# Kernel optimization log

Hardware: AMD Instinct MI355X
Metric: run time of the kernel (lower is better)

## Reference

```python
import jax, jax.numpy as jnp
import numpy as np

D_MODEL = 1024
N_HEADS = 16
D_K = D_MODEL // N_HEADS


def setup_inputs() -> dict:
    key = jax.random.key(0)
    k1, k2, k3, k4, k5 = jax.random.split(key, 5)
    B, S = 2, 2048
    scale = 1.0 / np.sqrt(D_MODEL)
    return {
        "query": jax.random.normal(k1, (B, S, D_MODEL), dtype=jnp.float32),
        "mask": jnp.ones((B, S, S), dtype=jnp.int32),
        "W_qkv": jax.random.normal(k2, (D_MODEL, 3 * D_MODEL), dtype=jnp.float32) * scale,
        "b_qkv": jax.random.normal(k3, (3 * D_MODEL,), dtype=jnp.float32) * 0.02,
        "W_out": jax.random.normal(k4, (D_MODEL, D_MODEL), dtype=jnp.float32) * scale,
        "b_out": jax.random.normal(k5, (D_MODEL,), dtype=jnp.float32) * 0.02,
    }


def reference(query, mask, W_qkv, b_qkv, W_out, b_out):
    B, S, _ = query.shape
    # fused QKV projection (all from query, matching the torch module)
    qkv = query @ W_qkv + b_qkv                      # [B, S, 3*D]
    q, k, v = jnp.split(qkv, 3, axis=-1)
    # [B, H, S, d_k]
    q = q.reshape(B, S, N_HEADS, D_K).transpose(0, 2, 1, 3)
    k = k.reshape(B, S, N_HEADS, D_K).transpose(0, 2, 1, 3)
    v = v.reshape(B, S, N_HEADS, D_K).transpose(0, 2, 1, 3)
    # scaled dot-product attention with explicit scores
    scores = jnp.einsum("bhqd,bhkd->bhqk", q, k) / jnp.sqrt(jnp.float32(D_K))
    m = mask[:, None, :, :]                           # [B, 1, S, S] broadcast over heads
    scores = jnp.where(m == 0, jnp.float32(-1e9), scores)
    attn = jax.nn.softmax(scores, axis=-1)           # dropout p=0 in eval -> identity
    ctx = jnp.einsum("bhqk,bhkd->bhqd", attn, v)     # [B, H, S, d_k]
    ctx = ctx.transpose(0, 2, 1, 3).reshape(B, S, D_MODEL)
    return ctx @ W_out + b_out
```

## Files before the change

kernel.cpp:

```cpp
#include <hip/hip_runtime.h>
#include <stdint.h>
#include <stddef.h>

#define S_LEN 2048
#define NB    2
#define DM    1024
#define NH    16
#define DKH   64
#define NTOK  4096
#define QKV_N 3072
#define QSCALE 0.18033688f

typedef __attribute__((ext_vector_type(4))) float floatx4;
using half2v = __attribute__((ext_vector_type(2))) _Float16;
using half4v = __attribute__((ext_vector_type(4))) _Float16;
using half8v = __attribute__((ext_vector_type(8))) _Float16;
using fp16x2 = __attribute__((ext_vector_type(2))) __fp16;

#if __has_builtin(__builtin_amdgcn_exp2f)
#define EXP2F __builtin_amdgcn_exp2f
#else
#define EXP2F exp2f
#endif

#define WAITCNT_VM8() asm volatile("s_waitcnt vmcnt(8)" ::: "memory")
#define WAITCNT_VM0() asm volatile("s_waitcnt vmcnt(0)" ::: "memory")
#define BARRIER_RAW() asm volatile("s_barrier" ::: "memory")

__device__ __forceinline__ void glds16(const void* g, void* l) {
    __builtin_amdgcn_global_load_lds((const __attribute__((address_space(1))) void*)g,
                                     (__attribute__((address_space(3))) void*)l,
                                     16, 0, 0);
}

__global__ __launch_bounds__(256) void prep_kernel(const float* __restrict__ query,
                                                   _Float16* __restrict__ qh,
                                                   const float* __restrict__ Wqkv,
                                                   _Float16* __restrict__ wqt,
                                                   const float* __restrict__ Wout,
                                                   _Float16* __restrict__ wot,
                                                   const int* __restrict__ mask,
                                                   int* __restrict__ flag) {
    __shared__ float tbuf[32][33];
    constexpr int CAST_B = NTOK * DM / 4 / 256;
    constexpr int TQ_B   = (QKV_N / 32) * (DM / 32);
    constexpr int TO_B   = (DM / 32) * (DM / 32);
    const int bid = blockIdx.x;

    if (bid < CAST_B) {
        int i = bid * 256 + threadIdx.x;
        float4 v = ((const float4*)query)[i];
        half4v o = {(_Float16)v.x, (_Float16)v.y, (_Float16)v.z, (_Float16)v.w};
        ((half4v*)qh)[i] = o;
    } else if (bid < CAST_B + TQ_B + TO_B) {
        const float* in; _Float16* out; int C, t;
        if (bid < CAST_B + TQ_B) { t = bid - CAST_B;        in = Wqkv; out = wqt; C = QKV_N; }
        else                     { t = bid - CAST_B - TQ_B; in = Wout; out = wot; C = DM;    }
        const int R = DM;
        int c0 = (t % (C / 32)) * 32, r0 = (t / (C / 32)) * 32;
        int x = threadIdx.x & 31, y0 = threadIdx.x >> 5;
        #pragma unroll
        for (int k = 0; k < 4; ++k) {
            int y = y0 + k * 8;
            tbuf[y][x] = in[(size_t)(r0 + y) * C + c0 + x];
        }
        __syncthreads();
        #pragma unroll
        for (int k = 0; k < 4; ++k) {
            int y = y0 + k * 8;
            out[(size_t)(c0 + y) * R + r0 + x] = (_Float16)tbuf[x][y];
        }
    } else {
        int i = (bid - CAST_B - TQ_B - TO_B) * 256 + threadIdx.x;
        int4 v = ((const int4*)mask)[i];
        if ((v.x == 0) | (v.y == 0) | (v.z == 0) | (v.w == 0)) *flag = 0;
    }
}

template <int FINAL, int BN>
__global__ __launch_bounds__(256) void gemm_bt_kernel(const _Float16* __restrict__ A,
                                                      const _Float16* __restrict__ Bt,
                                                      const float* __restrict__ bias,
                                                      float* __restrict__ Cf,
                                                      _Float16* __restrict__ Ch,
                                                      _Float16* __restrict__ Vt,
                                                      int M, int N, int K) {
    constexpr int NJ = BN / 32;
    __shared__ _Float16 As[128 * 64];
    __shared__ _Float16 Bs[BN * 64];

    const int nt = blockIdx.x, mt = blockIdx.y;
    const int tid = threadIdx.x, wave = tid >> 6, lane = tid & 63;
    const int quad = lane >> 4, l16 = lane & 15;
    const int wm = wave >> 1, wn = wave & 1;

    floatx4 acc[4][NJ];
    #pragma unroll
    for (int i = 0; i < 4; ++i)
        #pragma unroll
        for (int j = 0; j < NJ; ++j)
            #pragma unroll
            for (int r = 0; r < 4; ++r) acc[i][j][r] = 0.0f;

    const _Float16* Ab = A + (size_t)mt * 128 * K;
    const _Float16* Bb = Bt + (size_t)nt * BN * K;

    for (int kt = 0; kt < K; kt += 64) {
        #pragma unroll
        for (int p = 0; p < 4; ++p) {
            int slot = p * 256 + wave * 64 + lane;
            int row = slot >> 3, cc = slot & 7, c = cc ^ (row & 7);
            glds16(Ab + (size_t)row * K + kt + c * 8, As + (size_t)(p * 256 + wave * 64) * 8);
        }
        #pragma unroll
        for (int p = 0; p < BN / 32; ++p) {
            int slot = p * 256 + wave * 64 + lane;
            int row = slot >> 3, cc = slot & 7, c = cc ^ (row & 7);
            glds16(Bb + (size_t)row * K + kt + c * 8, Bs + (size_t)(p * 256 + wave * 64) * 8);
        }
        __syncthreads();

        #pragma unroll
        for (int kk = 0; kk < 2; ++kk) {
            half8v af[4], bfr[NJ];
            #pragma unroll
            for (int i = 0; i < 4; ++i) {
                int row = wm * 64 + i * 16 + l16;
                int c = (kk * 4 + quad) ^ (row & 7);
                af[i] = *(const half8v*)(As + row * 64 + c * 8);
            }
            #pragma unroll
            for (int j = 0; j < NJ; ++j) {
                int row = wn * (BN / 2) + j * 16 + l16;
                int c = (kk * 4 + quad) ^ (row & 7);
                bfr[j] = *(const half8v*)(Bs + row * 64 + c * 8);
            }
            #pragma unroll
            for (int i = 0; i < 4; ++i)
                #pragma unroll
                for (int j = 0; j < NJ; ++j)
                    acc[i][j] = __builtin_amdgcn_mfma_f32_16x16x32_f16(af[i], bfr[j], acc[i][j], 0, 0, 0);
        }
        __syncthreads();
    }

    #pragma unroll
    for (int j = 0; j < NJ; ++j) {
        int n = nt * BN + wn * (BN / 2) + j * 16 + l16;
        float bv = bias[n];
        #pragma unroll
        for (int i = 0; i < 4; ++i) {
            int m0 = mt * 128 + wm * 64 + i * 16 + quad * 4;
            float v[4];
            #pragma unroll
            for (int r = 0; r < 4; ++r) v[r] = acc[i][j][r] + bv;
            if (FINAL) {
                #pragma unroll
                for (int r = 0; r < 4; ++r) Cf[(size_t)(m0 + r) * N + n] = v[r];
            } else {
                if (n < DM) {
                    #pragma unroll
                    for (int r = 0; r < 4; ++r) v[r] *= QSCALE;
                }
                if (n < 2 * DM) {
                    #pragma unroll
                    for (int r = 0; r < 4; ++r)
                        Ch[(size_t)(m0 + r) * QKV_N + n] = (_Float16)v[r];
                } else {
                    int bb = m0 >> 11, s = m0 & (S_LEN - 1);
                    half4v t = {(_Float16)v[0], (_Float16)v[1], (_Float16)v[2], (_Float16)v[3]};
                    *(half4v*)(Vt + ((size_t)bb * (NH * DKH) + (n - 2 * DM)) * S_LEN + s) = t;
                }
            }
        }
    }
}

__global__ __launch_bounds__(256) void flash_kernel(const _Float16* __restrict__ qkv,
                                                    const _Float16* __restrict__ vt,
                                                    const int* __restrict__ mask,
                                                    const int* __restrict__ flag,
                                                    _Float16* __restrict__ ctx) {
    __shared__ _Float16 Ks[2 * 128 * 64];
    __shared__ _Float16 Vs[2 * 64 * 128];

    const int bh = blockIdx.x, qt = blockIdx.y;
    const int b = bh >> 4, h = bh & 15;
    const int tid = threadIdx.x, wave = tid >> 6, lane = tid & 63;
    const int quad = lane >> 4, l16 = lane & 15;
    const int allones = (*flag != 0);

    const _Float16* qrow0 = qkv + (size_t)(b * S_LEN + qt * 128 + wave * 32 + l16) * QKV_N + h * DKH;
    const _Float16* qrow1 = qrow0 + (size_t)16 * QKV_N;
    half8v qa0 = *(const half8v*)(qrow0 + quad * 8);
    half8v qa1 = *(const half8v*)(qrow0 + 32 + quad * 8);
    half8v qb0 = *(const half8v*)(qrow1 + quad * 8);
    half8v qb1 = *(const half8v*)(qrow1 + 32 + quad * 8);
    WAITCNT_VM0();

    const _Float16* kbase = qkv + (size_t)b * S_LEN * QKV_N + DM + h * DKH;
    const _Float16* vbase = vt + (size_t)(b * NH + h) * DKH * S_LEN;

    auto stage = [&](int buf, int kt) {
        #pragma unroll
        for (int p = 0; p < 4; ++p) {
            int slot = p * 256 + wave * 64 + lane;
            int row = slot >> 3, cc = slot & 7, c = cc ^ (row & 7);
            glds16(kbase + (size_t)(kt * 128 + row) * QKV_N + c * 8,
                   Ks + buf * (128 * 64) + (size_t)(p * 256 + wave * 64) * 8);
        }
        #pragma unroll
        for (int p = 0; p < 4; ++p) {
            int slot = p * 256 + wave * 64 + lane;
            int row = slot >> 4, cc = slot & 15, c = cc ^ (row & 15);
            glds16(vbase + (size_t)row * S_LEN + kt * 128 + c * 8,
                   Vs + buf * (64 * 128) + (size_t)(p * 256 + wave * 64) * 8);
        }
    };

    floatx4 oa[4], ob[4];
    #pragma unroll
    for (int c = 0; c < 4; ++c)
        #pragma unroll
        for (int r = 0; r < 4; ++r) { oa[c][r] = 0.0f; ob[c][r] = 0.0f; }
    float lsa = 0.0f, lsb = 0.0f;

    stage(0, 0);

    for (int kt = 0; kt < S_LEN / 128; ++kt) {
        const int cur = kt & 1;
        if (kt < S_LEN / 128 - 1) {
            stage(cur ^ 1, kt + 1);
            WAITCNT_VM8();
        } else {
            WAITCNT_VM0();
        }
        BARRIER_RAW();

        const _Float16* Ksb = Ks + cur * (128 * 64);
        const _Float16* Vsb = Vs + cur * (64 * 128);

        half4v pa[8], pb[8];
        #pragma unroll
        for (int j = 0; j < 8; ++j) {
            int rowk = j * 16 + l16;
            half8v a0 = *(const half8v*)(Ksb + rowk * 64 + ((quad) ^ (rowk & 7)) * 8);
            half8v a1 = *(const half8v*)(Ksb + rowk * 64 + ((4 + quad) ^ (rowk & 7)) * 8);
            floatx4 za, zb;
            #pragma unroll
            for (int r = 0; r < 4; ++r) { za[r] = 0.0f; zb[r] = 0.0f; }
            __builtin_amdgcn_s_setprio(1);
            za = __builtin_amdgcn_mfma_f32_16x16x32_f16(a0, qa0, za, 0, 0, 0);
            za = __builtin_amdgcn_mfma_f32_16x16x32_f16(a1, qa1, za, 0, 0, 0);
            zb = __builtin_amdgcn_mfma_f32_16x16x32_f16(a0, qb0, zb, 0, 0, 0);
            zb = __builtin_amdgcn_mfma_f32_16x16x32_f16(a1, qb1, zb, 0, 0, 0);
            __builtin_amdgcn_s_setprio(0);

            if (!allones) {
                for (int r = 0; r < 4; ++r) {
                    int s = kt * 128 + j * 16 + quad * 4 + r;
                    int qA = qt * 128 + wave * 32 + l16;
                    if (mask[((size_t)b * S_LEN + qA) * S_LEN + s] == 0) za[r] = -1e9f;
                    if (mask[((size_t)b * S_LEN + qA + 16) * S_LEN + s] == 0) zb[r] = -1e9f;
                }
            }

            float p0 = EXP2F(za[0]), p1 = EXP2F(za[1]), p2 = EXP2F(za[2]), p3 = EXP2F(za[3]);
            lsa += (p0 + p1) + (p2 + p3);
            fp16x2 lo = __builtin_amdgcn_cvt_pkrtz(p0, p1);
            fp16x2 hi = __builtin_amdgcn_cvt_pkrtz(p2, p3);
            half2v lo2 = __builtin_bit_cast(half2v, lo);
            half2v hi2 = __builtin_bit_cast(half2v, hi);
            half4v pka = {lo2.x, lo2.y, hi2.x, hi2.y};
            pa[j] = pka;

            p0 = EXP2F(zb[0]); p1 = EXP2F(zb[1]); p2 = EXP2F(zb[2]); p3 = EXP2F(zb[3]);
            lsb += (p0 + p1) + (p2 + p3);
            lo = __builtin_amdgcn_cvt_pkrtz(p0, p1);
            hi = __builtin_amdgcn_cvt_pkrtz(p2, p3);
            lo2 = __builtin_bit_cast(half2v, lo);
            hi2 = __builtin_bit_cast(half2v, hi);
            half4v pkb = {lo2.x, lo2.y, hi2.x, hi2.y};
            pb[j] = pkb;
        }

        #pragma unroll
        for (int j = 0; j < 8; ++j) {
            int g = 2 * j + (quad >> 1);
            __builtin_amdgcn_s_setprio(1);
            #pragma unroll
            for (int c = 0; c < 4; ++c) {
                int rowv = c * 16 + l16;
                half4v bv = *(const half4v*)(Vsb + rowv * 128 + ((g ^ (rowv & 15)) * 8) + (quad & 1) * 4);
                oa[c] = __builtin_amdgcn_mfma_f32_16x16x16f16(pa[j], bv, oa[c], 0, 0, 0);
                ob[c] = __builtin_amdgcn_mfma_f32_16x16x16f16(pb[j], bv, ob[c], 0, 0, 0);
            }
            __builtin_amdgcn_s_setprio(0);
        }

        if (kt < S_LEN / 128 - 1) BARRIER_RAW();
    }

    lsa += __shfl_xor(lsa, 16); lsa += __shfl_xor(lsa, 32);
    lsb += __shfl_xor(lsb, 16); lsb += __shfl_xor(lsb, 32);
    float lia[4], lib[4];
    #pragma unroll
    for (int r = 0; r < 4; ++r) {
        int src = (lane & 48) | ((lane >> 4) * 4 + r);
        lia[r] = 1.0f / __shfl(lsa, src);
        lib[r] = 1.0f / __shfl(lsb, src);
    }

    #pragma unroll
    for (int c = 0; c < 4; ++c)
        #pragma unroll
        for (int r = 0; r < 4; ++r) {
            int qA = qt * 128 + wave * 32 + quad * 4 + r;
            int col = h * DKH + c * 16 + l16;
            ctx[(size_t)(b * S_LEN + qA) * DM + col]      = (_Float16)(oa[c][r] * lia[r]);
            ctx[(size_t)(b * S_LEN + qA + 16) * DM + col] = (_Float16)(ob[c][r] * lib[r]);
        }
}

extern "C" void kernel_launch(void* const* d_in, const int* in_sizes, int n_in,
                              void* d_out, int out_size, void* d_ws, size_t ws_size,
                              hipStream_t stream) {
    const float* query = (const float*)d_in[0];
    const int*   mask  = (const int*)d_in[1];
    const float* W_qkv = (const float*)d_in[2];
    const float* b_qkv = (const float*)d_in[3];
    const float* W_out = (const float*)d_in[4];
    const float* b_out = (const float*)d_in[5];
    float* out = (float*)d_out;

    char* w = (char*)d_ws;
    _Float16* qh   = (_Float16*)w;  w += (size_t)NTOK * DM * 2;
    _Float16* wqt  = (_Float16*)w;  w += (size_t)QKV_N * DM * 2;
    _Float16* wot  = (_Float16*)w;  w += (size_t)DM * DM * 2;
    _Float16* qkvh = (_Float16*)w;  w += (size_t)NTOK * QKV_N * 2;
    _Float16* vt   = (_Float16*)w;  w += (size_t)NB * NH * DKH * S_LEN * 2;
    int*      flag = (int*)w;
    _Float16* ctxh = qh;

    hipMemsetAsync(flag, 1, 4, stream);

    constexpr int PREP_BLOCKS = (NTOK * DM / 4 / 256)
                              + (QKV_N / 32) * (DM / 32)
                              + (DM / 32) * (DM / 32)
                              + (NB * S_LEN * S_LEN / 4 / 256);
    prep_kernel<<<PREP_BLOCKS, 256, 0, stream>>>(query, qh, W_qkv, wqt, W_out, wot, mask, flag);

    gemm_bt_kernel<0, 128><<<dim3(QKV_N / 128, NTOK / 128), 256, 0, stream>>>(
        qh, wqt, b_qkv, nullptr, qkvh, vt, NTOK, QKV_N, DM);

    flash_kernel<<<dim3(NB * NH, S_LEN / 128), 256, 0, stream>>>(qkvh, vt, mask, flag, ctxh);

    gemm_bt_kernel<1, 64><<<dim3(DM / 64, NTOK / 128), 256, 0, stream>>>(
        ctxh, wot, b_out, out, nullptr, nullptr, NTOK, DM, DM);
}
```

Baseline: 213.3 us.

## Split flash attention work across 8 waves with 16 query rows each

The flash kernel moves from 4 waves handling 32 query rows each to 8 waves handling 16 rows each, with 512 threads per block. The K/V tile staging is spread over twice as many threads, so each thread issues half as many async loads, and the vmcnt wait is adjusted to match. The s_setprio hints are dropped. This aims to raise occupancy and latency hiding, at the cost of each wave reusing a K/V fragment for only one query tile instead of two, which doubles LDS reads per MFMA.

```diff
diff --git a/kernel.cpp b/kernel.cpp
--- a/kernel.cpp
+++ b/kernel.cpp
@@ -23,7 +23,7 @@
 #define EXP2F exp2f
 #endif
 
-#define WAITCNT_VM8() asm volatile("s_waitcnt vmcnt(8)" ::: "memory")
+#define WAITCNT_VM4() asm volatile("s_waitcnt vmcnt(4)" ::: "memory")
 #define WAITCNT_VM0() asm volatile("s_waitcnt vmcnt(0)" ::: "memory")
 #define BARRIER_RAW() asm volatile("s_barrier" ::: "memory")
 
@@ -176,11 +176,11 @@
     }
 }
 
-__global__ __launch_bounds__(256) void flash_kernel(const _Float16* __restrict__ qkv,
-                                                    const _Float16* __restrict__ vt,
-                                                    const int* __restrict__ mask,
-                                                    const int* __restrict__ flag,
-                                                    _Float16* __restrict__ ctx) {
+__global__ __launch_bounds__(512, 4) void flash_kernel(const _Float16* __restrict__ qkv,
+                                                       const _Float16* __restrict__ vt,
+                                                       const int* __restrict__ mask,
+                                                       const int* __restrict__ flag,
+                                                       _Float16* __restrict__ ctx) {
     __shared__ _Float16 Ks[2 * 128 * 64];
     __shared__ _Float16 Vs[2 * 64 * 128];
 
@@ -190,12 +190,9 @@
     const int quad = lane >> 4, l16 = lane & 15;
     const int allones = (*flag != 0);
 
-    const _Float16* qrow0 = qkv + (size_t)(b * S_LEN + qt * 128 + wave * 32 + l16) * QKV_N + h * DKH;
-    const _Float16* qrow1 = qrow0 + (size_t)16 * QKV_N;
+    const _Float16* qrow0 = qkv + (size_t)(b * S_LEN + qt * 128 + wave * 16 + l16) * QKV_N + h * DKH;
     half8v qa0 = *(const half8v*)(qrow0 + quad * 8);
     half8v qa1 = *(const half8v*)(qrow0 + 32 + quad * 8);
-    half8v qb0 = *(const half8v*)(qrow1 + quad * 8);
-    half8v qb1 = *(const half8v*)(qrow1 + 32 + quad * 8);
     WAITCNT_VM0();
 
     const _Float16* kbase = qkv + (size_t)b * S_LEN * QKV_N + DM + h * DKH;
@@ -203,27 +200,27 @@
 
     auto stage = [&](int buf, int kt) {
         #pragma unroll
-        for (int p = 0; p < 4; ++p) {
-            int slot = p * 256 + wave * 64 + lane;
+        for (int p = 0; p < 2; ++p) {
+            int slot = p * 512 + wave * 64 + lane;
             int row = slot >> 3, cc = slot & 7, c = cc ^ (row & 7);
             glds16(kbase + (size_t)(kt * 128 + row) * QKV_N + c * 8,
-                   Ks + buf * (128 * 64) + (size_t)(p * 256 + wave * 64) * 8);
-        }
-        #pragma unroll
-        for (int p = 0; p < 4; ++p) {
-            int slot = p * 256 + wave * 64 + lane;
+                   Ks + buf * (128 * 64) + (size_t)(p * 512 + wave * 64) * 8);
+        }
+        #pragma unroll
+        for (int p = 0; p < 2; ++p) {
+            int slot = p * 512 + wave * 64 + lane;
             int row = slot >> 4, cc = slot & 15, c = cc ^ (row & 15);
             glds16(vbase + (size_t)row * S_LEN + kt * 128 + c * 8,
-                   Vs + buf * (64 * 128) + (size_t)(p * 256 + wave * 64) * 8);
+                   Vs + buf * (64 * 128) + (size_t)(p * 512 + wave * 64) * 8);
         }
     };
 
-    floatx4 oa[4], ob[4];
+    floatx4 oa[4];
     #pragma unroll
     for (int c = 0; c < 4; ++c)
         #pragma unroll
-        for (int r = 0; r < 4; ++r) { oa[c][r] = 0.0f; ob[c][r] = 0.0f; }
-    float lsa = 0.0f, lsb = 0.0f;
+        for (int r = 0; r < 4; ++r) oa[c][r] = 0.0f;
+    float lsa = 0.0f;
 
     stage(0, 0);
 
@@ -231,7 +228,7 @@
         const int cur = kt & 1;
         if (kt < S_LEN / 128 - 1) {
             stage(cur ^ 1, kt + 1);
-            WAITCNT_VM8();
+            WAITCNT_VM4();
         } else {
             WAITCNT_VM0();
         }
@@ -240,28 +237,23 @@
         const _Float16* Ksb = Ks + cur * (128 * 64);
         const _Float16* Vsb = Vs + cur * (64 * 128);
 
-        half4v pa[8], pb[8];
+        half4v pa[8];
         #pragma unroll
         for (int j = 0; j < 8; ++j) {
             int rowk = j * 16 + l16;
             half8v a0 = *(const half8v*)(Ksb + rowk * 64 + ((quad) ^ (rowk & 7)) * 8);
             half8v a1 = *(const half8v*)(Ksb + rowk * 64 + ((4 + quad) ^ (rowk & 7)) * 8);
-            floatx4 za, zb;
-            #pragma unroll
-            for (int r = 0; r < 4; ++r) { za[r] = 0.0f; zb[r] = 0.0f; }
-            __builtin_amdgcn_s_setprio(1);
+            floatx4 za;
+            #pragma unroll
+            for (int r = 0; r < 4; ++r) za[r] = 0.0f;
             za = __builtin_amdgcn_mfma_f32_16x16x32_f16(a0, qa0, za, 0, 0, 0);
             za = __builtin_amdgcn_mfma_f32_16x16x32_f16(a1, qa1, za, 0, 0, 0);
-            zb = __builtin_amdgcn_mfma_f32_16x16x32_f16(a0, qb0, zb, 0, 0, 0);
-            zb = __builtin_amdgcn_mfma_f32_16x16x32_f16(a1, qb1, zb, 0, 0, 0);
-            __builtin_amdgcn_s_setprio(0);
 
             if (!allones) {
                 for (int r = 0; r < 4; ++r) {
                     int s = kt * 128 + j * 16 + quad * 4 + r;
-                    int qA = qt * 128 + wave * 32 + l16;
+                    int qA = qt * 128 + wave * 16 + l16;
                     if (mask[((size_t)b * S_LEN + qA) * S_LEN + s] == 0) za[r] = -1e9f;
-                    if (mask[((size_t)b * S_LEN + qA + 16) * S_LEN + s] == 0) zb[r] = -1e9f;
                 }
             }
 
@@ -273,52 +265,37 @@
             half2v hi2 = __builtin_bit_cast(half2v, hi);
             half4v pka = {lo2.x, lo2.y, hi2.x, hi2.y};
             pa[j] = pka;
-
-            p0 = EXP2F(zb[0]); p1 = EXP2F(zb[1]); p2 = EXP2F(zb[2]); p3 = EXP2F(zb[3]);
-            lsb += (p0 + p1) + (p2 + p3);
-            lo = __builtin_amdgcn_cvt_pkrtz(p0, p1);
-            hi = __builtin_amdgcn_cvt_pkrtz(p2, p3);
-            lo2 = __builtin_bit_cast(half2v, lo);
-            hi2 = __builtin_bit_cast(half2v, hi);
-            half4v pkb = {lo2.x, lo2.y, hi2.x, hi2.y};
-            pb[j] = pkb;
         }
 
         #pragma unroll
         for (int j = 0; j < 8; ++j) {
             int g = 2 * j + (quad >> 1);
-            __builtin_amdgcn_s_setprio(1);
             #pragma unroll
             for (int c = 0; c < 4; ++c) {
                 int rowv = c * 16 + l16;
                 half4v bv = *(const half4v*)(Vsb + rowv * 128 + ((g ^ (rowv & 15)) * 8) + (quad & 1) * 4);
                 oa[c] = __builtin_amdgcn_mfma_f32_16x16x16f16(pa[j], bv, oa[c], 0, 0, 0);
-                ob[c] = __builtin_amdgcn_mfma_f32_16x16x16f16(pb[j], bv, ob[c], 0, 0, 0);
-            }
-            __builtin_amdgcn_s_setprio(0);
+            }
         }
 
         if (kt < S_LEN / 128 - 1) BARRIER_RAW();
     }
 
     lsa += __shfl_xor(lsa, 16); lsa += __shfl_xor(lsa, 32);
-    lsb += __shfl_xor(lsb, 16); lsb += __shfl_xor(lsb, 32);
-    float lia[4], lib[4];
+    float lia[4];
     #pragma unroll
     for (int r = 0; r < 4; ++r) {
         int src = (lane & 48) | ((lane >> 4) * 4 + r);
         lia[r] = 1.0f / __shfl(lsa, src);
-        lib[r] = 1.0f / __shfl(lsb, src);
     }
 
     #pragma unroll
     for (int c = 0; c < 4; ++c)
         #pragma unroll
         for (int r = 0; r < 4; ++r) {
-            int qA = qt * 128 + wave * 32 + quad * 4 + r;
+            int qA = qt * 128 + wave * 16 + quad * 4 + r;
             int col = h * DKH + c * 16 + l16;
-            ctx[(size_t)(b * S_LEN + qA) * DM + col]      = (_Float16)(oa[c][r] * lia[r]);
-            ctx[(size_t)(b * S_LEN + qA + 16) * DM + col] = (_Float16)(ob[c][r] * lib[r]);
+            ctx[(size_t)(b * S_LEN + qA) * DM + col] = (_Float16)(oa[c][r] * lia[r]);
         }
 }
 
@@ -353,7 +330,7 @@
     gemm_bt_kernel<0, 128><<<dim3(QKV_N / 128, NTOK / 128), 256, 0, stream>>>(
         qh, wqt, b_qkv, nullptr, qkvh, vt, NTOK, QKV_N, DM);
 
-    flash_kernel<<<dim3(NB * NH, S_LEN / 128), 256, 0, stream>>>(qkvh, vt, mask, flag, ctxh);
+    flash_kernel<<<dim3(NB * NH, S_LEN / 128), 512, 0, stream>>>(qkvh, vt, mask, flag, ctxh);
 
     gemm_bt_kernel<1, 64><<<dim3(DM / 64, NTOK / 128), 256, 0, stream>>>(
         ctxh, wot, b_out, out, nullptr, nullptr, NTOK, DM, DM);
```

Result: no change. 209.9 us (-1.6%).

## Split flash attention key range across two wave groups with LDS reduction

Applied to the files above, without the earlier changes.

The flash kernel now runs 512 threads per block. Two groups of four waves each process half of the key sequence, using 64-key tiles with their own double-buffered K/V shared memory. After the loop, group 1 writes its partial output accumulators and row sums to LDS, and group 0 adds them in and writes the normalized context. This raises waves per block and parallelism per query tile, at the cost of an extra LDS reduction and barrier. The s_setprio hints were also removed.

```diff
diff --git a/kernel.cpp b/kernel.cpp
--- a/kernel.cpp
+++ b/kernel.cpp
@@ -23,7 +23,7 @@
 #define EXP2F exp2f
 #endif
 
-#define WAITCNT_VM8() asm volatile("s_waitcnt vmcnt(8)" ::: "memory")
+#define WAITCNT_VM4() asm volatile("s_waitcnt vmcnt(4)" ::: "memory")
 #define WAITCNT_VM0() asm volatile("s_waitcnt vmcnt(0)" ::: "memory")
 #define BARRIER_RAW() asm volatile("s_barrier" ::: "memory")
 
@@ -176,21 +176,23 @@
     }
 }
 
-__global__ __launch_bounds__(256) void flash_kernel(const _Float16* __restrict__ qkv,
-                                                    const _Float16* __restrict__ vt,
-                                                    const int* __restrict__ mask,
-                                                    const int* __restrict__ flag,
-                                                    _Float16* __restrict__ ctx) {
-    __shared__ _Float16 Ks[2 * 128 * 64];
-    __shared__ _Float16 Vs[2 * 64 * 128];
+__global__ __launch_bounds__(512, 4) void flash_kernel(const _Float16* __restrict__ qkv,
+                                                       const _Float16* __restrict__ vt,
+                                                       const int* __restrict__ mask,
+                                                       const int* __restrict__ flag,
+                                                       _Float16* __restrict__ ctx) {
+    __shared__ _Float16 Ks[2][2][64 * 64];
+    __shared__ _Float16 Vs[2][2][64 * 64];
 
     const int bh = blockIdx.x, qt = blockIdx.y;
     const int b = bh >> 4, h = bh & 15;
     const int tid = threadIdx.x, wave = tid >> 6, lane = tid & 63;
     const int quad = lane >> 4, l16 = lane & 15;
+    const int grp = wave >> 2;
+    const int w4 = wave & 3;
     const int allones = (*flag != 0);
 
-    const _Float16* qrow0 = qkv + (size_t)(b * S_LEN + qt * 128 + wave * 32 + l16) * QKV_N + h * DKH;
+    const _Float16* qrow0 = qkv + (size_t)(b * S_LEN + qt * 128 + w4 * 32 + l16) * QKV_N + h * DKH;
     const _Float16* qrow1 = qrow0 + (size_t)16 * QKV_N;
     half8v qa0 = *(const half8v*)(qrow0 + quad * 8);
     half8v qa1 = *(const half8v*)(qrow0 + 32 + quad * 8);
@@ -198,23 +200,23 @@
     half8v qb1 = *(const half8v*)(qrow1 + 32 + quad * 8);
     WAITCNT_VM0();
 
-    const _Float16* kbase = qkv + (size_t)b * S_LEN * QKV_N + DM + h * DKH;
-    const _Float16* vbase = vt + (size_t)(b * NH + h) * DKH * S_LEN;
+    const _Float16* kbase = qkv + (size_t)(b * S_LEN + grp * 1024) * QKV_N + DM + h * DKH;
+    const _Float16* vbase = vt + (size_t)(b * NH + h) * DKH * S_LEN + grp * 1024;
 
     auto stage = [&](int buf, int kt) {
         #pragma unroll
-        for (int p = 0; p < 4; ++p) {
-            int slot = p * 256 + wave * 64 + lane;
+        for (int p = 0; p < 2; ++p) {
+            int slot = p * 256 + w4 * 64 + lane;
             int row = slot >> 3, cc = slot & 7, c = cc ^ (row & 7);
-            glds16(kbase + (size_t)(kt * 128 + row) * QKV_N + c * 8,
-                   Ks + buf * (128 * 64) + (size_t)(p * 256 + wave * 64) * 8);
-        }
-        #pragma unroll
-        for (int p = 0; p < 4; ++p) {
-            int slot = p * 256 + wave * 64 + lane;
-            int row = slot >> 4, cc = slot & 15, c = cc ^ (row & 15);
-            glds16(vbase + (size_t)row * S_LEN + kt * 128 + c * 8,
-                   Vs + buf * (64 * 128) + (size_t)(p * 256 + wave * 64) * 8);
+            glds16(kbase + (size_t)(kt * 64 + row) * QKV_N + c * 8,
+                   &Ks[grp][buf][(p * 256 + w4 * 64) * 8]);
+        }
+        #pragma unroll
+        for (int p = 0; p < 2; ++p) {
+            int slot = p * 256 + w4 * 64 + lane;
+            int row = slot >> 3, cc = slot & 7, c = cc ^ (row & 7);
+            glds16(vbase + (size_t)row * S_LEN + kt * 64 + c * 8,
+                   &Vs[grp][buf][(p * 256 + w4 * 64) * 8]);
         }
     };
 
@@ -227,39 +229,37 @@
 
     stage(0, 0);
 
-    for (int kt = 0; kt < S_LEN / 128; ++kt) {
+    for (int kt = 0; kt < 16; ++kt) {
         const int cur = kt & 1;
-        if (kt < S_LEN / 128 - 1) {
+        if (kt < 15) {
             stage(cur ^ 1, kt + 1);
-            WAITCNT_VM8();
+            WAITCNT_VM4();
         } else {
             WAITCNT_VM0();
         }
         BARRIER_RAW();
 
-        const _Float16* Ksb = Ks + cur * (128 * 64);
-        const _Float16* Vsb = Vs + cur * (64 * 128);
-
-        half4v pa[8], pb[8];
-        #pragma unroll
-        for (int j = 0; j < 8; ++j) {
+        const _Float16* Ksb = Ks[grp][cur];
+        const _Float16* Vsb = Vs[grp][cur];
+
+        half4v pa[4], pb[4];
+        #pragma unroll
+        for (int j = 0; j < 4; ++j) {
             int rowk = j * 16 + l16;
             half8v a0 = *(const half8v*)(Ksb + rowk * 64 + ((quad) ^ (rowk & 7)) * 8);
             half8v a1 = *(const half8v*)(Ksb + rowk * 64 + ((4 + quad) ^ (rowk & 7)) * 8);
             floatx4 za, zb;
             #pragma unroll
             for (int r = 0; r < 4; ++r) { za[r] = 0.0f; zb[r] = 0.0f; }
-            __builtin_amdgcn_s_setprio(1);
             za = __builtin_amdgcn_mfma_f32_16x16x32_f16(a0, qa0, za, 0, 0, 0);
             za = __builtin_amdgcn_mfma_f32_16x16x32_f16(a1, qa1, za, 0, 0, 0);
             zb = __builtin_amdgcn_mfma_f32_16x16x32_f16(a0, qb0, zb, 0, 0, 0);
             zb = __builtin_amdgcn_mfma_f32_16x16x32_f16(a1, qb1, zb, 0, 0, 0);
-            __builtin_amdgcn_s_setprio(0);
 
             if (!allones) {
                 for (int r = 0; r < 4; ++r) {
-                    int s = kt * 128 + j * 16 + quad * 4 + r;
-                    int qA = qt * 128 + wave * 32 + l16;
+                    int s = grp * 1024 + kt * 64 + j * 16 + quad * 4 + r;
+                    int qA = qt * 128 + w4 * 32 + l16;
                     if (mask[((size_t)b * S_LEN + qA) * S_LEN + s] == 0) za[r] = -1e9f;
                     if (mask[((size_t)b * S_LEN + qA + 16) * S_LEN + s] == 0) zb[r] = -1e9f;
                 }
@@ -285,41 +285,66 @@
         }
 
         #pragma unroll
-        for (int j = 0; j < 8; ++j) {
-            int g = 2 * j + (quad >> 1);
-            __builtin_amdgcn_s_setprio(1);
+        for (int j = 0; j < 4; ++j) {
+            int g2 = 2 * j + (quad >> 1);
             #pragma unroll
             for (int c = 0; c < 4; ++c) {
                 int rowv = c * 16 + l16;
-                half4v bv = *(const half4v*)(Vsb + rowv * 128 + ((g ^ (rowv & 15)) * 8) + (quad & 1) * 4);
+                half4v bv = *(const half4v*)(Vsb + rowv * 64 + ((g2 ^ (rowv & 7)) * 8) + (quad & 1) * 4);
                 oa[c] = __builtin_amdgcn_mfma_f32_16x16x16f16(pa[j], bv, oa[c], 0, 0, 0);
                 ob[c] = __builtin_amdgcn_mfma_f32_16x16x16f16(pb[j], bv, ob[c], 0, 0, 0);
             }
-            __builtin_amdgcn_s_setprio(0);
-        }
-
-        if (kt < S_LEN / 128 - 1) BARRIER_RAW();
-    }
-
-    lsa += __shfl_xor(lsa, 16); lsa += __shfl_xor(lsa, 32);
-    lsb += __shfl_xor(lsb, 16); lsb += __shfl_xor(lsb, 32);
-    float lia[4], lib[4];
-    #pragma unroll
-    for (int r = 0; r < 4; ++r) {
-        int src = (lane & 48) | ((lane >> 4) * 4 + r);
-        lia[r] = 1.0f / __shfl(lsa, src);
-        lib[r] = 1.0f / __shfl(lsb, src);
-    }
-
-    #pragma unroll
-    for (int c = 0; c < 4; ++c)
+        }
+
+        if (kt < 15) BARRIER_RAW();
+    }
+
+    __syncthreads();
+    float* obuf = (float*)&Ks[0][0][0];
+    float* lbuf = (float*)&Vs[0][0][0];
+    if (grp == 1) {
+        #pragma unroll
+        for (int c = 0; c < 4; ++c)
+            #pragma unroll
+            for (int r = 0; r < 4; ++r) {
+                obuf[(w4 * 32 + (c * 4 + r)) * 64 + lane]      = oa[c][r];
+                obuf[(w4 * 32 + 16 + (c * 4 + r)) * 64 + lane] = ob[c][r];
+            }
+        lbuf[(w4 * 2 + 0) * 64 + lane] = lsa;
+        lbuf[(w4 * 2 + 1) * 64 + lane] = lsb;
+    }
+    __syncthreads();
+    if (grp == 0) {
+        #pragma unroll
+        for (int c = 0; c < 4; ++c)
+            #pragma unroll
+            for (int r = 0; r < 4; ++r) {
+                oa[c][r] += obuf[(w4 * 32 + (c * 4 + r)) * 64 + lane];
+                ob[c][r] += obuf[(w4 * 32 + 16 + (c * 4 + r)) * 64 + lane];
+            }
+        lsa += lbuf[(w4 * 2 + 0) * 64 + lane];
+        lsb += lbuf[(w4 * 2 + 1) * 64 + lane];
+
+        lsa += __shfl_xor(lsa, 16); lsa += __shfl_xor(lsa, 32);
+        lsb += __shfl_xor(lsb, 16); lsb += __shfl_xor(lsb, 32);
+        float lia[4], lib[4];
         #pragma unroll
         for (int r = 0; r < 4; ++r) {
-            int qA = qt * 128 + wave * 32 + quad * 4 + r;
-            int col = h * DKH + c * 16 + l16;
-            ctx[(size_t)(b * S_LEN + qA) * DM + col]      = (_Float16)(oa[c][r] * lia[r]);
-            ctx[(size_t)(b * S_LEN + qA + 16) * DM + col] = (_Float16)(ob[c][r] * lib[r]);
-        }
+            int src = (lane & 48) | ((lane >> 4) * 4 + r);
+            lia[r] = 1.0f / __shfl(lsa, src);
+            lib[r] = 1.0f / __shfl(lsb, src);
+        }
+
+        #pragma unroll
+        for (int c = 0; c < 4; ++c)
+            #pragma unroll
+            for (int r = 0; r < 4; ++r) {
+                int qA = qt * 128 + w4 * 32 + quad * 4 + r;
+                int col = h * DKH + c * 16 + l16;
+                ctx[(size_t)(b * S_LEN + qA) * DM + col]      = (_Float16)(oa[c][r] * lia[r]);
+                ctx[(size_t)(b * S_LEN + qA + 16) * DM + col] = (_Float16)(ob[c][r] * lib[r]);
+            }
+    }
 }
 
 extern "C" void kernel_launch(void* const* d_in, const int* in_sizes, int n_in,
@@ -353,7 +378,7 @@
     gemm_bt_kernel<0, 128><<<dim3(QKV_N / 128, NTOK / 128), 256, 0, stream>>>(
         qh, wqt, b_qkv, nullptr, qkvh, vt, NTOK, QKV_N, DM);
 
-    flash_kernel<<<dim3(NB * NH, S_LEN / 128), 256, 0, stream>>>(qkvh, vt, mask, flag, ctxh);
+    flash_kernel<<<dim3(NB * NH, S_LEN / 128), 512, 0, stream>>>(qkvh, vt, mask, flag, ctxh);
 
     gemm_bt_kernel<1, 64><<<dim3(DM / 64, NTOK / 128), 256, 0, stream>>>(
         ctxh, wot, b_out, out, nullptr, nullptr, NTOK, DM, DM);
```

Result: no change. 211.2 us, median of 2 (-1.0%).
